# Optimization experiments

Hardware: AMD Instinct MI355X
Metric: run time of the kernel (lower is better)

## Reference

```python
import jax, jax.numpy as jnp
import numpy as np

N_HEADS = 24
ROPE_BASE = 10000.0


def apply_rope(x, offset):
    """x: (B, H, L, Dh). Rotate pairs per RoPE (Su et al., 2021)."""
    B, H, L, Dh = x.shape
    inv_freq = 1.0 / (ROPE_BASE ** (jnp.arange(0, Dh, 2, dtype=jnp.float32) / Dh))  # (Dh/2,)
    t = jnp.arange(L, dtype=jnp.float32) + offset                                   # (L,)
    freqs = jnp.outer(t, inv_freq)                                                  # (L, Dh/2)
    emb = jnp.concatenate([freqs, freqs], axis=-1)                                  # (L, Dh)
    cos = jnp.cos(emb).astype(x.dtype)
    sin = jnp.sin(emb).astype(x.dtype)
    x1, x2 = x[..., : Dh // 2], x[..., Dh // 2 :]
    rotated = jnp.concatenate([-x2, x1], axis=-1)
    return x * cos + rotated * sin


def setup_inputs() -> dict:
    key = jax.random.key(0)
    k1, k2, k3 = jax.random.split(key, 3)
    B, L, D = 4, 2048, 1536
    x = jax.random.normal(k1, (B, L, D), dtype=jnp.float32)
    # Linear weights, torch convention (out_features, in_features), scaled init
    w_qkv = jax.random.normal(k2, (3 * D, D), dtype=jnp.float32) * 0.02
    w_out = jax.random.normal(k3, (D, D), dtype=jnp.float32) * 0.02
    return {"x": x, "w_qkv": w_qkv, "w_out": w_out, "pos_offset": 0}


def reference(x, w_qkv, w_out, pos_offset):
    B, L, D = x.shape
    H = N_HEADS
    Dh = D // H
    # fused QKV projection (no bias)
    qkv = jnp.einsum('bld,ed->ble', x, w_qkv)              # (B, L, 3D)
    qkv = qkv.reshape(B, L, 3, H, Dh)
    q = qkv[:, :, 0].transpose(0, 2, 1, 3)                 # (B, H, L, Dh)
    k = qkv[:, :, 1].transpose(0, 2, 1, 3)
    v = qkv[:, :, 2].transpose(0, 2, 1, 3)
    q = apply_rope(q, pos_offset)
    k = apply_rope(k, pos_offset)
    scale = 1.0 / np.sqrt(Dh)
    scores = jnp.einsum('bhqd,bhkd->bhqk', q, k) * scale   # (B, H, L, L)
    causal = jnp.tril(jnp.ones((L, L), dtype=bool))
    scores = jnp.where(causal, scores, jnp.finfo(scores.dtype).min)
    attn = jax.nn.softmax(scores, axis=-1)
    out = jnp.einsum('bhqk,bhkd->bhqd', attn, v)           # (B, H, L, Dh)
    out = out.transpose(0, 2, 1, 3).reshape(B, L, D)
    return jnp.einsum('bld,ed->ble', out, w_out)           # (B, L, D)
```

## Files before the change

### kernel.cpp

```cpp
#include <hip/hip_runtime.h>
#include <hip/hip_bf16.h>
#include <math.h>

typedef unsigned short u16;
typedef __bf16 b8 __attribute__((ext_vector_type(8)));
typedef __bf16 bf2t __attribute__((ext_vector_type(2)));
typedef float f4 __attribute__((ext_vector_type(4)));

#define B_ 4
#define L_ 2048
#define D_ 1536
#define H_ 24
#define DH_ 64

__device__ __forceinline__ float bf2f(u16 v) {
    union { unsigned u; float f; } z; z.u = ((unsigned)v) << 16; return z.f;
}
__device__ __forceinline__ u16 f2bf(float f) {
    union { float f; unsigned u; } z; z.f = f;
    unsigned u = z.u;
    return (u16)((u + 0x7fffu + ((u >> 16) & 1u)) >> 16);
}
__device__ __forceinline__ void f4_to_bf4(f4 v, u16 o[4]) {
#if __has_builtin(__builtin_amdgcn_cvt_pk_bf16_f32)
    union { bf2t b; unsigned u; } z0, z1;
    z0.b = __builtin_amdgcn_cvt_pk_bf16_f32(v[0], v[1]);
    z1.b = __builtin_amdgcn_cvt_pk_bf16_f32(v[2], v[3]);
    o[0] = (u16)(z0.u & 0xffffu); o[1] = (u16)(z0.u >> 16);
    o[2] = (u16)(z1.u & 0xffffu); o[3] = (u16)(z1.u >> 16);
#else
    o[0] = f2bf(v[0]); o[1] = f2bf(v[1]); o[2] = f2bf(v[2]); o[3] = f2bf(v[3]);
#endif
}

__global__ __launch_bounds__(256) void cvt_f32_bf16(const float* __restrict__ src,
                                                    u16* __restrict__ dst, int n4) {
    int i = blockIdx.x * 256 + threadIdx.x;
    if (i >= n4) return;
    float4 vv = ((const float4*)src)[i];
    f4 v = {vv.x, vv.y, vv.z, vv.w};
    u16 o4[4];
    f4_to_bf4(v, o4);
    ushort4 o = {o4[0], o4[1], o4[2], o4[3]};
    ((ushort4*)dst)[i] = o;
}

__global__ __launch_bounds__(256) void gemm128(const u16* __restrict__ A,
                                               const u16* __restrict__ B,
                                               float* __restrict__ Cf,
                                               u16* __restrict__ Qp,
                                               u16* __restrict__ Kp,
                                               u16* __restrict__ Vp,
                                               int M, int N, int K, int mode) {
    __shared__ u16 As[128 * 32];
    __shared__ u16 Bs[128 * 32];
    const int tid = threadIdx.x;
    const int wave = tid >> 6, lane = tid & 63;
    const int m16 = lane & 15, quad = lane >> 4;
    const int bm = blockIdx.y * 128, bn = blockIdx.x * 128;
    const int wr = (wave >> 1) * 64, wc = (wave & 1) * 64;

    f4 acc[4][4];
#pragma unroll
    for (int i = 0; i < 4; i++)
#pragma unroll
        for (int j = 0; j < 4; j++) acc[i][j] = (f4)0.0f;

    const int c0 = wave * 64 + lane;
    const int r0 = c0 >> 2, col0 = (c0 & 3) * 8;
    const int c1 = c0 + 256;
    const int r1 = c1 >> 2, col1 = (c1 & 3) * 8;

    for (int k0 = 0; k0 < K; k0 += 32) {
        __syncthreads();
        __builtin_amdgcn_global_load_lds(
            (const __attribute__((address_space(1))) void*)(A + (size_t)(bm + r0) * K + k0 + col0),
            (__attribute__((address_space(3))) void*)(As + (size_t)c0 * 8), 16, 0, 0);
        __builtin_amdgcn_global_load_lds(
            (const __attribute__((address_space(1))) void*)(A + (size_t)(bm + r1) * K + k0 + col1),
            (__attribute__((address_space(3))) void*)(As + (size_t)c1 * 8), 16, 0, 0);
        __builtin_amdgcn_global_load_lds(
            (const __attribute__((address_space(1))) void*)(B + (size_t)(bn + r0) * K + k0 + col0),
            (__attribute__((address_space(3))) void*)(Bs + (size_t)c0 * 8), 16, 0, 0);
        __builtin_amdgcn_global_load_lds(
            (const __attribute__((address_space(1))) void*)(B + (size_t)(bn + r1) * K + k0 + col1),
            (__attribute__((address_space(3))) void*)(Bs + (size_t)c1 * 8), 16, 0, 0);
        __syncthreads();
        b8 af[4], bfm[4];
#pragma unroll
        for (int i = 0; i < 4; i++) af[i] = *(const b8*)(As + (wr + i * 16 + m16) * 32 + quad * 8);
#pragma unroll
        for (int j = 0; j < 4; j++) bfm[j] = *(const b8*)(Bs + (wc + j * 16 + m16) * 32 + quad * 8);
#pragma unroll
        for (int i = 0; i < 4; i++)
#pragma unroll
            for (int j = 0; j < 4; j++)
                acc[i][j] = __builtin_amdgcn_mfma_f32_16x16x32_bf16(af[i], bfm[j], acc[i][j], 0, 0, 0);
    }

    if (mode == 0) {
#pragma unroll
        for (int i = 0; i < 4; i++)
#pragma unroll
            for (int j = 0; j < 4; j++)
#pragma unroll
                for (int r = 0; r < 4; r++) {
                    int row = bm + wr + i * 16 + quad * 4 + r;
                    int col = bn + wc + j * 16 + m16;
                    Cf[(size_t)row * N + col] = acc[i][j][r];
                }
    } else {
#pragma unroll
        for (int j = 0; j < 4; j++) {
            const int colbase = bn + wc + j * 16;
            const int s = colbase / D_;
            const int h = (colbase % D_) / DH_;
            const int dh0 = colbase % DH_;
            u16* dst = (s == 0) ? Qp : ((s == 1) ? Kp : Vp);
#pragma unroll
            for (int i = 0; i < 4; i++) {
                u16 o4[4];
                f4_to_bf4(acc[i][j], o4);
#pragma unroll
                for (int r = 0; r < 4; r++) {
                    int row = bm + wr + i * 16 + quad * 4 + r;
                    int b = row >> 11, l = row & (L_ - 1);
                    dst[((size_t)(b * H_ + h) * L_ + l) * DH_ + dh0 + m16] = o4[r];
                }
            }
        }
    }
}

__global__ __launch_bounds__(256) void rope_inplace(u16* __restrict__ Qp,
                                                    u16* __restrict__ Kp,
                                                    const int* __restrict__ pos) {
    unsigned idx = blockIdx.x * 256 + threadIdx.x;
    int i = idx & 31;
    unsigned t1 = idx >> 5;
    int l = t1 & (L_ - 1);
    unsigned t2 = t1 >> 11;
    int h = t2 % H_;
    int b = t2 / H_;
    float t = (float)(l + pos[0]);
    float invf = powf(10000.0f, -(float)(2 * i) * (1.0f / 64.0f));
    float ang = t * invf;
    float c = cosf(ang), s = sinf(ang);
    size_t base = ((size_t)(b * H_ + h) * L_ + l) * DH_;
    {
        float x1 = bf2f(Qp[base + i]), x2 = bf2f(Qp[base + i + 32]);
        Qp[base + i] = f2bf((x1 * c - x2 * s) * 0.125f);
        Qp[base + i + 32] = f2bf((x2 * c + x1 * s) * 0.125f);
    }
    {
        float x1 = bf2f(Kp[base + i]), x2 = bf2f(Kp[base + i + 32]);
        Kp[base + i] = f2bf(x1 * c - x2 * s);
        Kp[base + i + 32] = f2bf(x2 * c + x1 * s);
    }
}

__global__ __launch_bounds__(256, 3) void attn(const u16* __restrict__ Q,
                                               const u16* __restrict__ K,
                                               const u16* __restrict__ V,
                                               u16* __restrict__ O) {
    __shared__ u16 Ks[64 * 72];
    __shared__ u16 Vs[64 * 72];
    __shared__ u16 Ps[4][32 * 72];
    const int tid = threadIdx.x;
    const int wave = tid >> 6, lane = tid & 63;
    const int m16 = lane & 15, quad = lane >> 4;
    const int bh = blockIdx.y;
    const int tA = blockIdx.x;
    const int tB = 15 - tA;
    const int qA = tA * 128 + wave * 32;
    const int qB = tB * 128 + wave * 32;
    const int srow = tid >> 2, scol = (tid & 3) * 16, g = (tid & 3);

    b8 qfA[2][2], qfB[2][2];
#pragma unroll
    for (int i = 0; i < 2; i++) {
        const u16* qa = Q + ((size_t)bh * L_ + qA + i * 16 + m16) * DH_;
        qfA[i][0] = *(const b8*)(qa + quad * 8);
        qfA[i][1] = *(const b8*)(qa + 32 + quad * 8);
        const u16* qb = Q + ((size_t)bh * L_ + qB + i * 16 + m16) * DH_;
        qfB[i][0] = *(const b8*)(qb + quad * 8);
        qfB[i][1] = *(const b8*)(qb + 32 + quad * 8);
    }

    float lrA[2][4], lrB[2][4];
    f4 oaccA[2][4], oaccB[2][4];
#pragma unroll
    for (int i = 0; i < 2; i++)
#pragma unroll
        for (int r = 0; r < 4; r++) { lrA[i][r] = 0.0f; lrB[i][r] = 0.0f; }
#pragma unroll
    for (int i = 0; i < 2; i++)
#pragma unroll
        for (int n = 0; n < 4; n++) { oaccA[i][n] = (f4)0.0f; oaccB[i][n] = (f4)0.0f; }

    u16* pw = Ps[wave];

    auto process = [&](int qw, b8 (&qf)[2][2], float (&lrow)[2][4], f4 (&oacc)[2][4],
                       int kbase) {
        const bool need_mask = (kbase + 64 > qw);
        f4 s[2][4];
#pragma unroll
        for (int sub = 0; sub < 4; sub++) {
            b8 k0 = *(const b8*)(Ks + (sub * 16 + m16) * 72 + quad * 8);
            b8 k1 = *(const b8*)(Ks + (sub * 16 + m16) * 72 + 32 + quad * 8);
#pragma unroll
            for (int i = 0; i < 2; i++) {
                f4 c = (f4)0.0f;
                c = __builtin_amdgcn_mfma_f32_16x16x32_bf16(qf[i][0], k0, c, 0, 0, 0);
                c = __builtin_amdgcn_mfma_f32_16x16x32_bf16(qf[i][1], k1, c, 0, 0, 0);
                s[i][sub] = c;
            }
        }
        if (need_mask) {
#pragma unroll
            for (int i = 0; i < 2; i++)
#pragma unroll
                for (int sub = 0; sub < 4; sub++)
#pragma unroll
                    for (int r = 0; r < 4; r++) {
                        const int key = kbase + sub * 16 + m16;
                        const int qg = qw + i * 16 + quad * 4 + r;
                        float p = __expf(s[i][sub][r]);
                        p = (key <= qg) ? p : 0.0f;
                        s[i][sub][r] = p;
                        lrow[i][r] += p;
                    }
        } else {
#pragma unroll
            for (int i = 0; i < 2; i++)
#pragma unroll
                for (int sub = 0; sub < 4; sub++)
#pragma unroll
                    for (int r = 0; r < 4; r++) {
                        float p = __expf(s[i][sub][r]);
                        s[i][sub][r] = p;
                        lrow[i][r] += p;
                    }
        }
#pragma unroll
        for (int i = 0; i < 2; i++)
#pragma unroll
            for (int sub = 0; sub < 4; sub++) {
                u16 o4[4];
                f4_to_bf4(s[i][sub], o4);
#pragma unroll
                for (int r = 0; r < 4; r++)
                    pw[(i * 16 + quad * 4 + r) * 72 + sub * 16 + m16] = o4[r];
            }
#pragma unroll
        for (int ks = 0; ks < 2; ks++) {
            b8 pf[2];
#pragma unroll
            for (int i = 0; i < 2; i++)
                pf[i] = *(const b8*)(pw + (i * 16 + m16) * 72 + ks * 32 + quad * 8);
#pragma unroll
            for (int n = 0; n < 4; n++) {
                b8 vf = *(const b8*)(Vs + (n * 16 + m16) * 72 +
                                     ((ks * 32 + quad * 8 + n * 16) & 63));
#pragma unroll
                for (int i = 0; i < 2; i++)
                    oacc[i][n] = __builtin_amdgcn_mfma_f32_16x16x32_bf16(pf[i], vf, oacc[i][n], 0, 0, 0);
            }
        }
    };

    const int nkt = 2 * tB + 2;
    for (int kt = 0; kt < nkt; kt++) {
        const int kbase = kt * 64;
        __syncthreads();
        {
            const u16* kg = K + ((size_t)bh * L_ + kbase + srow) * DH_ + scol;
            uint4 a0 = *(const uint4*)kg;
            uint4 a1 = *(const uint4*)(kg + 8);
            const u16* vg = V + ((size_t)bh * L_ + kbase + srow) * DH_ + scol;
            uint4 b0 = *(const uint4*)vg;
            uint4 b1 = *(const uint4*)(vg + 8);
            *(uint4*)(Ks + srow * 72 + scol) = a0;
            *(uint4*)(Ks + srow * 72 + scol + 8) = a1;
            u16 tmp[16];
            *(uint4*)(tmp) = b0;
            *(uint4*)(tmp + 8) = b1;
#pragma unroll
            for (int e = 0; e < 16; e++)
                Vs[(scol + e) * 72 + ((srow + g * 16) & 63)] = tmp[e];
        }
        __syncthreads();
        if (kbase <= qA + 31) process(qA, qfA, lrA, oaccA, kbase);
        if (kbase <= qB + 31) process(qB, qfB, lrB, oaccB, kbase);
    }

#pragma unroll
    for (int x = 1; x < 16; x <<= 1)
#pragma unroll
        for (int i = 0; i < 2; i++)
#pragma unroll
            for (int r = 0; r < 4; r++) {
                lrA[i][r] += __shfl_xor(lrA[i][r], x, 64);
                lrB[i][r] += __shfl_xor(lrB[i][r], x, 64);
            }
    const int b = bh / H_, h = bh % H_;
#pragma unroll
    for (int i = 0; i < 2; i++)
#pragma unroll
        for (int r = 0; r < 4; r++) {
            const float invA = 1.0f / lrA[i][r];
            const float invB = 1.0f / lrB[i][r];
            const int qa = qA + i * 16 + quad * 4 + r;
            const int qb = qB + i * 16 + quad * 4 + r;
#pragma unroll
            for (int n = 0; n < 4; n++) {
                O[((size_t)(b * L_ + qa)) * D_ + h * 64 + n * 16 + m16] = f2bf(oaccA[i][n][r] * invA);
                O[((size_t)(b * L_ + qb)) * D_ + h * 64 + n * 16 + m16] = f2bf(oaccB[i][n][r] * invB);
            }
        }
}

extern "C" void kernel_launch(void* const* d_in, const int* in_sizes, int n_in,
                              void* d_out, int out_size, void* d_ws, size_t ws_size,
                              hipStream_t stream) {
    const float* x = (const float*)d_in[0];
    const float* w_qkv = (const float*)d_in[1];
    const float* w_out = (const float*)d_in[2];
    const int* pos = (const int*)d_in[3];
    float* out = (float*)d_out;

    const size_t nx = (size_t)B_ * L_ * D_;
    const size_t nwq = (size_t)3 * D_ * D_;
    const size_t nwo = (size_t)D_ * D_;
    const size_t per = (size_t)B_ * H_ * L_ * DH_;

    u16* xb = (u16*)d_ws;
    u16* wqkvb = xb + nx;
    u16* woutb = wqkvb + nwq;
    u16* Qp = woutb + nwo;
    u16* Kp = Qp + per;
    u16* Vp = Kp + per;
    u16* aO = xb;

    cvt_f32_bf16<<<(int)((nx / 4 + 255) / 256), 256, 0, stream>>>(x, xb, (int)(nx / 4));
    cvt_f32_bf16<<<(int)((nwq / 4 + 255) / 256), 256, 0, stream>>>(w_qkv, wqkvb, (int)(nwq / 4));
    cvt_f32_bf16<<<(int)((nwo / 4 + 255) / 256), 256, 0, stream>>>(w_out, woutb, (int)(nwo / 4));

    gemm128<<<dim3(3 * D_ / 128, B_ * L_ / 128), 256, 0, stream>>>(
        xb, wqkvb, nullptr, Qp, Kp, Vp, B_ * L_, 3 * D_, D_, 1);
    rope_inplace<<<(B_ * H_ * L_ * 32) / 256, 256, 0, stream>>>(Qp, Kp, pos);
    attn<<<dim3(L_ / 256, B_ * H_), 256, 0, stream>>>(Qp, Kp, Vp, aO);
    gemm128<<<dim3(D_ / 128, B_ * L_ / 128), 256, 0, stream>>>(
        aO, woutb, out, nullptr, nullptr, nullptr, B_ * L_, D_, D_, 0);
}
```

Before: 526.5 us.

## Fuse RoPE into QKV GEMM epilogue, merge conversions, deepen GEMM K tile

Removes the separate RoPE kernel and instead applies the rotation and the query scaling directly on the accumulators in the QKV GEMM epilogue. Each wave's 64 columns map to exactly one head, so its x1/x2 halves come from the j and j+2 fragments. The three fp32-to-bf16 conversion launches become one kernel that indexes into the contiguous workspace. The GEMM K step grows from 32 to 64 with a doubled LDS tile, which halves the barrier count per tile. Costs are more LDS per block, fast __sincosf in place of precise sinf and cosf, and trig recomputed per element inside the epilogue.

```diff
diff --git a/kernel.cpp b/kernel.cpp
--- a/kernel.cpp
+++ b/kernel.cpp
@@ -33,11 +33,19 @@
 #endif
 }
 
-__global__ __launch_bounds__(256) void cvt_f32_bf16(const float* __restrict__ src,
-                                                    u16* __restrict__ dst, int n4) {
+__global__ __launch_bounds__(256) void cvt3(const float* __restrict__ x,
+                                            const float* __restrict__ wq,
+                                            const float* __restrict__ wo,
+                                            u16* __restrict__ dst,
+                                            int n4x, int n4q, int n4t) {
     int i = blockIdx.x * 256 + threadIdx.x;
-    if (i >= n4) return;
-    float4 vv = ((const float4*)src)[i];
+    if (i >= n4t) return;
+    const float* src;
+    int idx;
+    if (i < n4x) { src = x; idx = i; }
+    else if (i < n4x + n4q) { src = wq; idx = i - n4x; }
+    else { src = wo; idx = i - n4x - n4q; }
+    float4 vv = ((const float4*)src)[idx];
     f4 v = {vv.x, vv.y, vv.z, vv.w};
     u16 o4[4];
     f4_to_bf4(v, o4);
@@ -51,9 +59,10 @@
                                                u16* __restrict__ Qp,
                                                u16* __restrict__ Kp,
                                                u16* __restrict__ Vp,
+                                               const int* __restrict__ pos,
                                                int M, int N, int K, int mode) {
-    __shared__ u16 As[128 * 32];
-    __shared__ u16 Bs[128 * 32];
+    __shared__ u16 As[128 * 64];
+    __shared__ u16 Bs[128 * 64];
     const int tid = threadIdx.x;
     const int wave = tid >> 6, lane = tid & 63;
     const int m16 = lane & 15, quad = lane >> 4;
@@ -66,36 +75,42 @@
 #pragma unroll
         for (int j = 0; j < 4; j++) acc[i][j] = (f4)0.0f;
 
-    const int c0 = wave * 64 + lane;
-    const int r0 = c0 >> 2, col0 = (c0 & 3) * 8;
-    const int c1 = c0 + 256;
-    const int r1 = c1 >> 2, col1 = (c1 & 3) * 8;
-
-    for (int k0 = 0; k0 < K; k0 += 32) {
+    int crow[4], ccol[4];
+#pragma unroll
+    for (int i = 0; i < 4; i++) {
+        int c = tid + 256 * i;
+        crow[i] = c >> 3;
+        ccol[i] = (c & 7) * 8;
+    }
+
+    for (int k0 = 0; k0 < K; k0 += 64) {
         __syncthreads();
-        __builtin_amdgcn_global_load_lds(
-            (const __attribute__((address_space(1))) void*)(A + (size_t)(bm + r0) * K + k0 + col0),
-            (__attribute__((address_space(3))) void*)(As + (size_t)c0 * 8), 16, 0, 0);
-        __builtin_amdgcn_global_load_lds(
-            (const __attribute__((address_space(1))) void*)(A + (size_t)(bm + r1) * K + k0 + col1),
-            (__attribute__((address_space(3))) void*)(As + (size_t)c1 * 8), 16, 0, 0);
-        __builtin_amdgcn_global_load_lds(
-            (const __attribute__((address_space(1))) void*)(B + (size_t)(bn + r0) * K + k0 + col0),
-            (__attribute__((address_space(3))) void*)(Bs + (size_t)c0 * 8), 16, 0, 0);
-        __builtin_amdgcn_global_load_lds(
-            (const __attribute__((address_space(1))) void*)(B + (size_t)(bn + r1) * K + k0 + col1),
-            (__attribute__((address_space(3))) void*)(Bs + (size_t)c1 * 8), 16, 0, 0);
+#pragma unroll
+        for (int i = 0; i < 4; i++)
+            __builtin_amdgcn_global_load_lds(
+                (const __attribute__((address_space(1))) void*)(A + (size_t)(bm + crow[i]) * K + k0 + ccol[i]),
+                (__attribute__((address_space(3))) void*)(As + (size_t)(tid + 256 * i) * 8), 16, 0, 0);
+#pragma unroll
+        for (int i = 0; i < 4; i++)
+            __builtin_amdgcn_global_load_lds(
+                (const __attribute__((address_space(1))) void*)(B + (size_t)(bn + crow[i]) * K + k0 + ccol[i]),
+                (__attribute__((address_space(3))) void*)(Bs + (size_t)(tid + 256 * i) * 8), 16, 0, 0);
         __syncthreads();
-        b8 af[4], bfm[4];
-#pragma unroll
-        for (int i = 0; i < 4; i++) af[i] = *(const b8*)(As + (wr + i * 16 + m16) * 32 + quad * 8);
-#pragma unroll
-        for (int j = 0; j < 4; j++) bfm[j] = *(const b8*)(Bs + (wc + j * 16 + m16) * 32 + quad * 8);
-#pragma unroll
-        for (int i = 0; i < 4; i++)
+#pragma unroll
+        for (int kk = 0; kk < 2; kk++) {
+            b8 af[4], bfm[4];
+#pragma unroll
+            for (int i = 0; i < 4; i++)
+                af[i] = *(const b8*)(As + (wr + i * 16 + m16) * 64 + kk * 32 + quad * 8);
 #pragma unroll
             for (int j = 0; j < 4; j++)
-                acc[i][j] = __builtin_amdgcn_mfma_f32_16x16x32_bf16(af[i], bfm[j], acc[i][j], 0, 0, 0);
+                bfm[j] = *(const b8*)(Bs + (wc + j * 16 + m16) * 64 + kk * 32 + quad * 8);
+#pragma unroll
+            for (int i = 0; i < 4; i++)
+#pragma unroll
+                for (int j = 0; j < 4; j++)
+                    acc[i][j] = __builtin_amdgcn_mfma_f32_16x16x32_bf16(af[i], bfm[j], acc[i][j], 0, 0, 0);
+        }
     }
 
     if (mode == 0) {
@@ -110,52 +125,48 @@
                     Cf[(size_t)row * N + col] = acc[i][j][r];
                 }
     } else {
-#pragma unroll
-        for (int j = 0; j < 4; j++) {
-            const int colbase = bn + wc + j * 16;
-            const int s = colbase / D_;
-            const int h = (colbase % D_) / DH_;
-            const int dh0 = colbase % DH_;
-            u16* dst = (s == 0) ? Qp : ((s == 1) ? Kp : Vp);
-#pragma unroll
-            for (int i = 0; i < 4; i++) {
-                u16 o4[4];
-                f4_to_bf4(acc[i][j], o4);
-#pragma unroll
-                for (int r = 0; r < 4; r++) {
-                    int row = bm + wr + i * 16 + quad * 4 + r;
-                    int b = row >> 11, l = row & (L_ - 1);
-                    dst[((size_t)(b * H_ + h) * L_ + l) * DH_ + dh0 + m16] = o4[r];
+        const int cb = bn + wc;
+        const int s = cb / D_;
+        const int h = (cb % D_) / DH_;
+        u16* dst = (s == 0) ? Qp : ((s == 1) ? Kp : Vp);
+        if (s == 2) {
+#pragma unroll
+            for (int j = 0; j < 4; j++)
+#pragma unroll
+                for (int i = 0; i < 4; i++) {
+                    u16 o4[4];
+                    f4_to_bf4(acc[i][j], o4);
+#pragma unroll
+                    for (int r = 0; r < 4; r++) {
+                        int row = bm + wr + i * 16 + quad * 4 + r;
+                        int b = row >> 11, l = row & (L_ - 1);
+                        dst[((size_t)(b * H_ + h) * L_ + l) * DH_ + j * 16 + m16] = o4[r];
+                    }
                 }
-            }
-        }
-    }
-}
-
-__global__ __launch_bounds__(256) void rope_inplace(u16* __restrict__ Qp,
-                                                    u16* __restrict__ Kp,
-                                                    const int* __restrict__ pos) {
-    unsigned idx = blockIdx.x * 256 + threadIdx.x;
-    int i = idx & 31;
-    unsigned t1 = idx >> 5;
-    int l = t1 & (L_ - 1);
-    unsigned t2 = t1 >> 11;
-    int h = t2 % H_;
-    int b = t2 / H_;
-    float t = (float)(l + pos[0]);
-    float invf = powf(10000.0f, -(float)(2 * i) * (1.0f / 64.0f));
-    float ang = t * invf;
-    float c = cosf(ang), s = sinf(ang);
-    size_t base = ((size_t)(b * H_ + h) * L_ + l) * DH_;
-    {
-        float x1 = bf2f(Qp[base + i]), x2 = bf2f(Qp[base + i + 32]);
-        Qp[base + i] = f2bf((x1 * c - x2 * s) * 0.125f);
-        Qp[base + i + 32] = f2bf((x2 * c + x1 * s) * 0.125f);
-    }
-    {
-        float x1 = bf2f(Kp[base + i]), x2 = bf2f(Kp[base + i + 32]);
-        Kp[base + i] = f2bf(x1 * c - x2 * s);
-        Kp[base + i + 32] = f2bf(x2 * c + x1 * s);
+        } else {
+            const int pos0 = *pos;
+            const float qscale = (s == 0) ? 0.125f : 1.0f;
+#pragma unroll
+            for (int p = 0; p < 2; p++) {
+                const float invf = powf(10000.0f, -(float)(2 * (p * 16 + m16)) * (1.0f / 64.0f));
+#pragma unroll
+                for (int i = 0; i < 4; i++)
+#pragma unroll
+                    for (int r = 0; r < 4; r++) {
+                        int row = bm + wr + i * 16 + quad * 4 + r;
+                        int b = row >> 11, l = row & (L_ - 1);
+                        float ang = (float)(l + pos0) * invf;
+                        float sn, cs;
+                        __sincosf(ang, &sn, &cs);
+                        float x1 = acc[i][p][r], x2 = acc[i][p + 2][r];
+                        float o1 = (x1 * cs - x2 * sn) * qscale;
+                        float o2 = (x2 * cs + x1 * sn) * qscale;
+                        size_t base = ((size_t)(b * H_ + h) * L_ + l) * DH_ + p * 16 + m16;
+                        dst[base] = f2bf(o1);
+                        dst[base + 32] = f2bf(o2);
+                    }
+            }
+        }
     }
 }
 
@@ -342,14 +353,13 @@
     u16* Vp = Kp + per;
     u16* aO = xb;
 
-    cvt_f32_bf16<<<(int)((nx / 4 + 255) / 256), 256, 0, stream>>>(x, xb, (int)(nx / 4));
-    cvt_f32_bf16<<<(int)((nwq / 4 + 255) / 256), 256, 0, stream>>>(w_qkv, wqkvb, (int)(nwq / 4));
-    cvt_f32_bf16<<<(int)((nwo / 4 + 255) / 256), 256, 0, stream>>>(w_out, woutb, (int)(nwo / 4));
+    const int n4x = (int)(nx / 4), n4q = (int)(nwq / 4), n4o = (int)(nwo / 4);
+    const int n4t = n4x + n4q + n4o;
+    cvt3<<<(n4t + 255) / 256, 256, 0, stream>>>(x, w_qkv, w_out, xb, n4x, n4q, n4t);
 
     gemm128<<<dim3(3 * D_ / 128, B_ * L_ / 128), 256, 0, stream>>>(
-        xb, wqkvb, nullptr, Qp, Kp, Vp, B_ * L_, 3 * D_, D_, 1);
-    rope_inplace<<<(B_ * H_ * L_ * 32) / 256, 256, 0, stream>>>(Qp, Kp, pos);
+        xb, wqkvb, nullptr, Qp, Kp, Vp, pos, B_ * L_, 3 * D_, D_, 1);
     attn<<<dim3(L_ / 256, B_ * H_), 256, 0, stream>>>(Qp, Kp, Vp, aO);
     gemm128<<<dim3(D_ / 128, B_ * L_ / 128), 256, 0, stream>>>(
-        aO, woutb, out, nullptr, nullptr, nullptr, B_ * L_, D_, D_, 0);
-}
+        aO, woutb, out, nullptr, nullptr, nullptr, nullptr, B_ * L_, D_, D_, 0);
+}
```

Result: slower. 654.3 us (+24.3%).
